# Kernel tuning notes

Measured on AMD Instinct MI355X. Metric: run time of the kernel, lower is better.

## Reference

```python
import jax, jax.numpy as jnp
import numpy as np

N = 100000   # nodes
E = 300000   # directed edges
NG = 4096    # graphs in batch
F_IN = 22
HID = 128


def setup_inputs() -> dict:
    key = jax.random.key(0)
    ks = jax.random.split(key, 32)
    s = 0.05
    inp = {
        "x": jax.random.normal(ks[0], (N, F_IN), jnp.float32),
        "edge_index": jax.random.randint(ks[1], (2, E), 0, N),
        "batch": jnp.sort(jax.random.randint(ks[2], (N,), 0, NG)),
        # GAT layer 1: 22 -> 4 heads x 32
        "W1": jax.random.normal(ks[3], (F_IN, HID), jnp.float32) * s,
        "as1": jax.random.normal(ks[4], (4, 32), jnp.float32) * s,
        "ad1": jax.random.normal(ks[5], (4, 32), jnp.float32) * s,
        "b1": jnp.zeros((HID,), jnp.float32),
        "g1": jnp.ones((HID,), jnp.float32),
        "be1": jnp.zeros((HID,), jnp.float32),
        # GAT layer 2: 128 -> 4 heads x 32
        "W2": jax.random.normal(ks[6], (HID, HID), jnp.float32) * s,
        "as2": jax.random.normal(ks[7], (4, 32), jnp.float32) * s,
        "ad2": jax.random.normal(ks[8], (4, 32), jnp.float32) * s,
        "b2": jnp.zeros((HID,), jnp.float32),
        "g2": jnp.ones((HID,), jnp.float32),
        "be2": jnp.zeros((HID,), jnp.float32),
        # GAT layer 3: 128 -> 1 head x 128
        "W3": jax.random.normal(ks[9], (HID, HID), jnp.float32) * s,
        "as3": jax.random.normal(ks[10], (1, HID), jnp.float32) * s,
        "ad3": jax.random.normal(ks[11], (1, HID), jnp.float32) * s,
        "b3": jnp.zeros((HID,), jnp.float32),
        "g3": jnp.ones((HID,), jnp.float32),
        "be3": jnp.zeros((HID,), jnp.float32),
        # MLP head
        "fw1": jax.random.normal(ks[12], (HID, 64), jnp.float32) * s,
        "fb1": jnp.zeros((64,), jnp.float32),
        "fw2": jax.random.normal(ks[13], (64, 1), jnp.float32) * s,
        "fb2": jnp.zeros((1,), jnp.float32),
    }
    return inp


def reference(x, edge_index, batch, W1, as1, ad1, b1, g1, be1,
              W2, as2, ad2, b2, g2, be2, W3, as3, ad3, b3, g3, be3,
              fw1, fb1, fw2, fb2):
    n = x.shape[0]
    sl = jnp.arange(n)
    src = jnp.concatenate([edge_index[0], sl])  # PyG GATConv adds self-loops
    dst = jnp.concatenate([edge_index[1], sl])

    def gat(h_in, W, a_s, a_d, b):
        H, C = a_s.shape
        h = (h_in @ W).reshape(n, H, C)                      # [N,H,C]
        al_s = jnp.einsum('nhc,hc->nh', h, a_s)              # per-node src score
        al_d = jnp.einsum('nhc,hc->nh', h, a_d)
        e = jax.nn.leaky_relu(al_s[src] + al_d[dst], 0.2)    # [Etot,H]
        emax = jax.ops.segment_max(e, dst, num_segments=n)
        ex = jnp.exp(e - emax[dst])
        den = jax.ops.segment_sum(ex, dst, num_segments=n)
        alpha = ex / (den[dst] + 1e-16)                       # segment softmax over in-edges
        msg = h[src] * alpha[:, :, None]                      # [Etot,H,C]
        out = jax.ops.segment_sum(msg, dst, num_segments=n)
        return out.reshape(n, H * C) + b

    def bn(h, g, be):
        m = h.mean(0)
        v = h.var(0)
        return (h - m) * jax.lax.rsqrt(v + 1e-5) * g + be

    h = jax.nn.relu(bn(gat(x, W1, as1, ad1, b1), g1, be1))
    h = jax.nn.relu(bn(gat(h, W2, as2, ad2, b2), g2, be2))
    h = jax.nn.relu(bn(gat(h, W3, as3, ad3, b3), g3, be3))

    # global mean pool over graphs
    s = jax.ops.segment_sum(h, batch, num_segments=NG)
    cnt = jax.ops.segment_sum(jnp.ones((n,), h.dtype), batch, num_segments=NG)
    pooled = s / jnp.maximum(cnt, 1.0)[:, None]

    z = jax.nn.relu(pooled @ fw1 + fb1)
    return z @ fw2 + fb2
```

## Files before the change

kernel.cpp:

```cpp
#include <hip/hip_runtime.h>

#define N_NODES 100000
#define N_EDGES 300000
#define N_ETOT  400000
#define NGRAPH  4096
#define HID     128
#define NBLK_SCAN 391
#define PNPB    32
#define STATS_BLOCKS 512
#define NSLICE  16

typedef __attribute__((ext_vector_type(8))) short short8;
typedef __attribute__((ext_vector_type(8))) ushort ushort8;
typedef __attribute__((ext_vector_type(4))) float f32x4;

__device__ __forceinline__ ushort f2bf(float f) {
    union { float f; unsigned u; } x; x.f = f;
    unsigned r = x.u + 0x7FFF + ((x.u >> 16) & 1);
    return (ushort)(r >> 16);
}

__device__ __forceinline__ float bf2f(ushort v) {
    union { unsigned u; float f; } t;
    t.u = ((unsigned)v) << 16;
    return t.f;
}

__device__ __forceinline__ float2 bf2f2(unsigned v) {
    union { unsigned u; float f; } lo, hi;
    lo.u = v << 16;
    hi.u = v & 0xFFFF0000u;
    return make_float2(lo.f, hi.f);
}

#define SETUP_W      36864
#define SETUP_SUMS   (SETUP_W + 3 * NSLICE * 256)
#define SETUP_CNTS   (SETUP_SUMS + N_NODES)
#define SETUP_TOT    (SETUP_CNTS + NGRAPH * HID + NGRAPH)
__global__ __launch_bounds__(256) void setup_kernel(
    const float* __restrict__ W1, const float* __restrict__ W2, const float* __restrict__ W3,
    ushort* __restrict__ Wt1, ushort* __restrict__ Wt2, ushort* __restrict__ Wt3,
    float* __restrict__ sums_base, int* __restrict__ counts,
    float* __restrict__ pooled)
{
    const int i = blockIdx.x * 256 + threadIdx.x;
    if (i < 16384) {
        int c = i >> 7, k = i & 127;
        Wt2[c * 128 + k] = f2bf(W2[k * 128 + c]);
    } else if (i < 32768) {
        int j = i - 16384; int c = j >> 7, k = j & 127;
        Wt3[c * 128 + k] = f2bf(W3[k * 128 + c]);
    } else if (i < SETUP_W) {
        int j = i - 32768; int c = j >> 5, k = j & 31;
        Wt1[c * 32 + k] = (k < 22) ? f2bf(W1[k * 128 + c]) : (ushort)0;
    } else if (i < SETUP_SUMS) {
        sums_base[i - SETUP_W] = 0.f;
    } else if (i < SETUP_CNTS) {
        counts[i - SETUP_SUMS] = 0;
    } else if (i < SETUP_TOT) {
        pooled[i - SETUP_CNTS] = 0.f;
    }
}

template<int K, bool PRE_BN, int HH, bool DX>
__global__ __launch_bounds__(256) void mfma_gemm_kernel(
    const ushort* __restrict__ Ab, const float* __restrict__ Af,
    const ushort* __restrict__ Wt,
    const float* __restrict__ sums, const float* __restrict__ g, const float* __restrict__ be,
    const float* __restrict__ avs, const float* __restrict__ avd,
    ushort* __restrict__ Cb, float* __restrict__ als, float* __restrict__ ald, int M)
{
    constexpr int SEGS = K / 8;
    constexpr int SSH  = (K == 128) ? 4 : 2;
    constexpr int SWM  = SEGS - 1;
    constexpr int NPB  = SEGS / 2;
    constexpr int KT   = K / 32;

    __shared__ ushort Bsm[128 * K];
    __shared__ float scsh[256];

    const int tid  = threadIdx.x;
    const int wave = tid >> 6;
    const int lane = tid & 63;
    const int ln   = lane & 15;
    const int quad = lane >> 4;
    const int r0   = blockIdx.x * 64 + wave * 16;
    const int ra   = r0 + ln;

    short8 wR[NPB];
    #pragma unroll
    for (int q = 0; q < NPB; ++q) {
        const int chunk = tid + q * 256;
        const int r   = chunk >> SSH;
        const int seg = chunk & SWM;
        wR[q] = *(const short8*)&Wt[(size_t)r * K + seg * 8];
    }
    short8 aF[KT];
    #pragma unroll
    for (int kt = 0; kt < KT; ++kt) {
        if constexpr (DX) {
            const int rr = min(ra, N_NODES - 1);
            #pragma unroll
            for (int i = 0; i < 8; ++i) {
                const int c = kt * 32 + quad * 8 + i;
                const float f = (c < 22) ? Af[(size_t)rr * 22 + c] : 0.f;
                aF[kt][i] = (short)f2bf(f);
            }
        } else {
            aF[kt] = *(const short8*)&Ab[(size_t)ra * K + kt * 32 + quad * 8];
        }
    }
    if constexpr (PRE_BN) {
        if (tid < 128) {
            float s = 0.f, q2 = 0.f;
            for (int b = 0; b < NSLICE; ++b) {
                s  += sums[b * 256 + tid];
                q2 += sums[b * 256 + 128 + tid];
            }
            const float m  = s * (1.f / N_NODES);
            const float v  = q2 * (1.f / N_NODES) - m * m;
            const float sc = g[tid] * rsqrtf(v + 1e-5f);
            scsh[tid]       = sc;
            scsh[tid + 128] = be[tid] - m * sc;
        }
    }
    #pragma unroll
    for (int q = 0; q < NPB; ++q) {
        const int chunk = tid + q * 256;
        const int r   = chunk >> SSH;
        const int seg = chunk & SWM;
        const int sp  = seg ^ (r & SWM);
        *(short8*)&Bsm[r * K + sp * 8] = wR[q];
    }
    __syncthreads();

    if constexpr (PRE_BN) {
        #pragma unroll
        for (int kt = 0; kt < KT; ++kt) {
            const int c0 = kt * 32 + quad * 8;
            #pragma unroll
            for (int i = 0; i < 8; ++i) {
                float f = bf2f((ushort)aF[kt][i]);
                f = fmaxf(f * scsh[c0 + i] + scsh[128 + c0 + i], 0.f);
                aF[kt][i] = (short)f2bf(f);
            }
        }
    }

    f32x4 acc[8] = {};
    #pragma unroll
    for (int kt = 0; kt < KT; ++kt) {
        #pragma unroll
        for (int tc = 0; tc < 8; ++tc) {
            const int ca = tc * 16 + ln;
            const short8 b = *(const short8*)&Bsm[ca * K + (((kt * 4 + quad) ^ (ca & SWM)) * 8)];
            acc[tc] = __builtin_amdgcn_mfma_f32_16x16x32_bf16(aF[kt], b, acc[tc], 0, 0, 0);
        }
    }

    #pragma unroll
    for (int rg = 0; rg < 4; ++rg) {
        const int gr = r0 + quad * 4 + rg;
        if (gr < M) {
            #pragma unroll
            for (int tc = 0; tc < 8; ++tc)
                Cb[(size_t)gr * HID + tc * 16 + ln] = f2bf(acc[tc][rg]);
        }
    }

    float avsr[8], avdr[8];
    #pragma unroll
    for (int tc = 0; tc < 8; ++tc) {
        avsr[tc] = avs[tc * 16 + ln];
        avdr[tc] = avd[tc * 16 + ln];
    }
    #pragma unroll
    for (int rg = 0; rg < 4; ++rg) {
        const int gr = r0 + quad * 4 + rg;
        float s[4], d[4];
        #pragma unroll
        for (int h = 0; h < 4; ++h) {
            float sv = 0.f, dv = 0.f;
            sv += acc[2 * h][rg] * avsr[2 * h];
            sv += acc[2 * h + 1][rg] * avsr[2 * h + 1];
            dv += acc[2 * h][rg] * avdr[2 * h];
            dv += acc[2 * h + 1][rg] * avdr[2 * h + 1];
            s[h] = sv; d[h] = dv;
        }
        #pragma unroll
        for (int m = 1; m < 16; m <<= 1) {
            #pragma unroll
            for (int h = 0; h < 4; ++h) {
                s[h] += __shfl_xor(s[h], m);
                d[h] += __shfl_xor(d[h], m);
            }
        }
        if (ln == 0 && gr < M) {
            if (HH == 4) {
                #pragma unroll
                for (int h = 0; h < 4; ++h) {
                    als[gr * 4 + h] = s[h];
                    ald[gr * 4 + h] = d[h];
                }
            } else {
                als[gr] = ((s[0] + s[1]) + s[2]) + s[3];
                ald[gr] = ((d[0] + d[1]) + d[2]) + d[3];
            }
        }
    }
}

__global__ void hist_kernel(const int* __restrict__ ei, int* __restrict__ counts) {
    int e = blockIdx.x * blockDim.x + threadIdx.x;
    if (e >= N_ETOT) return;
    int dst = (e < N_EDGES) ? ei[N_EDGES + e] : e - N_EDGES;
    atomicAdd(&counts[dst], 1);
}

__global__ __launch_bounds__(256) void scanA_kernel(
    const int* __restrict__ counts, int* __restrict__ rowptr, int* __restrict__ bsum)
{
    __shared__ int ls[256];
    const int t = threadIdx.x;
    const int i = blockIdx.x * 256 + t;
    const int v = (i < N_NODES) ? counts[i] : 0;
    ls[t] = v; __syncthreads();
    #pragma unroll
    for (int off = 1; off < 256; off <<= 1) {
        int add = (t >= off) ? ls[t - off] : 0;
        __syncthreads();
        ls[t] += add;
        __syncthreads();
    }
    if (i < N_NODES) rowptr[i] = ls[t] - v;
    if (t == 255) bsum[blockIdx.x] = ls[255];
}

__global__ __launch_bounds__(256) void scanC_kernel(
    int* __restrict__ rowptr, const int* __restrict__ bsum, int* __restrict__ cursor)
{
    __shared__ int red[256];
    const int t = threadIdx.x;
    int s = 0;
    for (int b = t; b < (int)blockIdx.x; b += 256) s += bsum[b];
    red[t] = s;
    __syncthreads();
    #pragma unroll
    for (int off = 128; off; off >>= 1) {
        if (t < off) red[t] += red[t + off];
        __syncthreads();
    }
    const int base = red[0];
    const int i = blockIdx.x * 256 + t;
    if (i < N_NODES) {
        const int v = rowptr[i] + base;
        rowptr[i] = v;
        cursor[i] = v;
    }
    if (i == 0) rowptr[N_NODES] = N_ETOT;
}

__global__ void scatter_kernel(const int* __restrict__ ei, int* __restrict__ cursor,
                               int* __restrict__ psrc)
{
    int e = blockIdx.x * blockDim.x + threadIdx.x;
    if (e >= N_ETOT) return;
    int src, dst;
    if (e < N_EDGES) { src = ei[e]; dst = ei[N_EDGES + e]; }
    else             { src = dst = e - N_EDGES; }
    int pos = atomicAdd(&cursor[dst], 1);
    psrc[pos] = src;
}

template<int HH>
__global__ __launch_bounds__(256) void agg_kernel(
    const ushort* __restrict__ H, const float* __restrict__ als,
    const float* __restrict__ ald, const int* __restrict__ rowptr,
    const int* __restrict__ psrc, ushort* __restrict__ Outb)
{
    const int tid   = threadIdx.x;
    const int w     = tid >> 6;
    const int lane  = tid & 63;
    const int grp   = lane >> 4;
    const int cl    = lane & 15;
    const int hd    = (HH == 4) ? (cl >> 2) : 0;
    const int nodeA = blockIdx.x * 8 + w * 2;
    const int nodeB = nodeA + 1;

    const int r0A = rowptr[nodeA];
    const int r1A = rowptr[nodeA + 1];
    const int r1B = rowptr[nodeB + 1];
    const float aldA = (HH == 4) ? ald[nodeA * 4 + hd] : ald[nodeA];
    const float aldB = (HH == 4) ? ald[nodeB * 4 + hd] : ald[nodeB];

    float denA = 0.f, denB = 0.f;
    float accA[8] = {}, accB[8] = {};
    int pA = r0A + grp;
    int pB = r1A + grp;
    bool aA = pA < r1A;
    bool aB = pB < r1B;
    int sA = psrc[aA ? pA : (r1A - 1)];
    int sB = psrc[aB ? pB : (r1B - 1)];
    while (pA < r1A || pB < r1B) {
        const float svA = (HH == 4) ? als[sA * 4 + hd] : als[sA];
        const float svB = (HH == 4) ? als[sB * 4 + hd] : als[sB];
        const uint4 hvA = *(const uint4*)&H[(size_t)sA * HID + cl * 8];
        const uint4 hvB = *(const uint4*)&H[(size_t)sB * HID + cl * 8];
        const int pA2 = pA + 4, pB2 = pB + 4;
        const bool aA2 = pA2 < r1A;
        const bool aB2 = pB2 < r1B;
        const int sA2 = psrc[aA2 ? pA2 : (r1A - 1)];
        const int sB2 = psrc[aB2 ? pB2 : (r1B - 1)];

        float vA = svA + aldA; vA = (vA > 0.f) ? vA : 0.2f * vA;
        float vB = svB + aldB; vB = (vB > 0.f) ? vB : 0.2f * vB;
        const float exA = aA ? __expf(vA) : 0.f;
        const float exB = aB ? __expf(vB) : 0.f;
        {
            const float2 h0 = bf2f2(hvA.x), h1 = bf2f2(hvA.y);
            const float2 h2 = bf2f2(hvA.z), h3 = bf2f2(hvA.w);
            accA[0] += exA * h0.x; accA[1] += exA * h0.y;
            accA[2] += exA * h1.x; accA[3] += exA * h1.y;
            accA[4] += exA * h2.x; accA[5] += exA * h2.y;
            accA[6] += exA * h3.x; accA[7] += exA * h3.y;
            denA += exA;
        }
        {
            const float2 h0 = bf2f2(hvB.x), h1 = bf2f2(hvB.y);
            const float2 h2 = bf2f2(hvB.z), h3 = bf2f2(hvB.w);
            accB[0] += exB * h0.x; accB[1] += exB * h0.y;
            accB[2] += exB * h1.x; accB[3] += exB * h1.y;
            accB[4] += exB * h2.x; accB[5] += exB * h2.y;
            accB[6] += exB * h3.x; accB[7] += exB * h3.y;
            denB += exB;
        }
        pA = pA2; pB = pB2;
        aA = aA2; aB = aB2;
        sA = sA2; sB = sB2;
    }
    #pragma unroll
    for (int m = 16; m < 64; m <<= 1) {
        denA += __shfl_xor(denA, m);
        denB += __shfl_xor(denB, m);
        #pragma unroll
        for (int i = 0; i < 8; ++i) {
            accA[i] += __shfl_xor(accA[i], m);
            accB[i] += __shfl_xor(accB[i], m);
        }
    }
    if (grp == 0) {
        const float inv = 1.f / (denA + 1e-16f);
        ushort8 o;
        #pragma unroll
        for (int i = 0; i < 8; ++i) o[i] = f2bf(accA[i] * inv);
        *(ushort8*)&Outb[(size_t)nodeA * HID + cl * 8] = o;
    } else if (grp == 1) {
        const float inv = 1.f / (denB + 1e-16f);
        ushort8 o;
        #pragma unroll
        for (int i = 0; i < 8; ++i) o[i] = f2bf(accB[i] * inv);
        *(ushort8*)&Outb[(size_t)nodeB * HID + cl * 8] = o;
    }
}

__global__ __launch_bounds__(256) void bn_stats_kernel(
    const ushort* __restrict__ X, float* __restrict__ sums_sl)
{
    __shared__ float ls[16][128], lq[16][128];
    const int tid = threadIdx.x;
    const int ro  = tid >> 4;
    const int ci  = tid & 15;
    const int c0  = ci * 8;
    const int rpb = (N_NODES + STATS_BLOCKS - 1) / STATS_BLOCKS;
    const int r0  = blockIdx.x * rpb;
    const int r1  = min(r0 + rpb, N_NODES);

    float s[8] = {}, q[8] = {};
    for (int r = r0 + ro; r < r1; r += 16) {
        const ushort8 v = *(const ushort8*)&X[(size_t)r * HID + c0];
        #pragma unroll
        for (int j = 0; j < 8; ++j) {
            const float f = bf2f(v[j]);
            s[j] += f; q[j] += f * f;
        }
    }
    #pragma unroll
    for (int j = 0; j < 8; ++j) { ls[ro][c0 + j] = s[j]; lq[ro][c0 + j] = q[j]; }
    __syncthreads();
    const int half = tid >> 7;
    const int c    = tid & 127;
    float acc = 0.f;
    if (half == 0) {
        #pragma unroll
        for (int k = 0; k < 16; ++k) acc += ls[k][c];
    } else {
        #pragma unroll
        for (int k = 0; k < 16; ++k) acc += lq[k][c];
    }
    atomicAdd(&sums_sl[(blockIdx.x & (NSLICE - 1)) * 256 + tid], acc);
}

__global__ __launch_bounds__(128) void bn_pool_kernel(
    const ushort* __restrict__ X,
    const float* __restrict__ sums, const float* __restrict__ g, const float* __restrict__ be,
    const int* __restrict__ batch, float* __restrict__ pooled, float* __restrict__ cnt)
{
    const int c = threadIdx.x;
    float s = 0.f, q2 = 0.f;
    for (int b = 0; b < NSLICE; ++b) {
        s  += sums[b * 256 + c];
        q2 += sums[b * 256 + 128 + c];
    }
    const float m  = s * (1.f / N_NODES);
    const float vv = q2 * (1.f / N_NODES) - m * m;
    const float sc = g[c] * rsqrtf(vv + 1e-5f);
    const float sh = be[c] - m * sc;

    const int n0 = blockIdx.x * PNPB;
    const int n1 = min(n0 + PNPB, N_NODES);
    int gcur = batch[n0];
    float acc = 0.f;
    int run = 0;
    for (int n = n0; n < n1; ++n) {
        const int gg = batch[n];
        if (gg != gcur) {
            atomicAdd(&pooled[(size_t)gcur * HID + c], acc);
            if (c == 0) atomicAdd(&cnt[gcur], (float)run);
            acc = 0.f; run = 0; gcur = gg;
        }
        const float v = bf2f(X[(size_t)n * HID + c]) * sc + sh;
        acc += fmaxf(v, 0.f);
        ++run;
    }
    atomicAdd(&pooled[(size_t)gcur * HID + c], acc);
    if (c == 0) atomicAdd(&cnt[gcur], (float)run);
}

__global__ __launch_bounds__(256) void mlp_kernel(
    const float* __restrict__ pooled, const float* __restrict__ cnt,
    const float* __restrict__ fw1, const float* __restrict__ fb1,
    const float* __restrict__ fw2, const float* __restrict__ fb2,
    float* __restrict__ out)
{
    __shared__ float w1[HID * 64];
    __shared__ float rows[4][HID];
    const int tid = threadIdx.x;
    for (int i = tid; i < HID * 64; i += 256) w1[i] = fw1[i];
    const int gl = tid >> 6;
    const int j  = tid & 63;
    const float b1 = fb1[j];
    const float w2 = fw2[j];
    __syncthreads();
    #pragma unroll
    for (int it = 0; it < 4; ++it) {
        const int g = blockIdx.x * 16 + it * 4 + gl;
        const float inv = 1.f / fmaxf(cnt[g], 1.f);
        rows[gl][j]      = pooled[(size_t)g * HID + j] * inv;
        rows[gl][j + 64] = pooled[(size_t)g * HID + 64 + j] * inv;
        __syncthreads();
        float z = b1;
        #pragma unroll 8
        for (int c2 = 0; c2 < HID; ++c2) z += rows[gl][c2] * w1[c2 * 64 + j];
        z = fmaxf(z, 0.f);
        float p = z * w2;
        #pragma unroll
        for (int off = 32; off; off >>= 1) p += __shfl_down(p, off);
        if (j == 0) out[g] = p + fb2[0];
        __syncthreads();
    }
}

extern "C" void kernel_launch(void* const* d_in, const int* in_sizes, int n_in,
                              void* d_out, int out_size, void* d_ws, size_t ws_size,
                              hipStream_t stream)
{
    const float* x     = (const float*)d_in[0];
    const int*   ei    = (const int*)d_in[1];
    const int*   batch = (const int*)d_in[2];
    const float* W1  = (const float*)d_in[3];
    const float* as1 = (const float*)d_in[4];
    const float* ad1 = (const float*)d_in[5];
    const float* g1  = (const float*)d_in[7];
    const float* be1 = (const float*)d_in[8];
    const float* W2  = (const float*)d_in[9];
    const float* as2 = (const float*)d_in[10];
    const float* ad2 = (const float*)d_in[11];
    const float* g2  = (const float*)d_in[13];
    const float* be2 = (const float*)d_in[14];
    const float* W3  = (const float*)d_in[15];
    const float* as3 = (const float*)d_in[16];
    const float* ad3 = (const float*)d_in[17];
    const float* g3  = (const float*)d_in[19];
    const float* be3 = (const float*)d_in[20];
    const float* fw1 = (const float*)d_in[21];
    const float* fb1 = (const float*)d_in[22];
    const float* fw2 = (const float*)d_in[23];
    const float* fb2 = (const float*)d_in[24];
    float* out = (float*)d_out;

    ushort* Hb  = (ushort*)d_ws;
    ushort* Bh  = Hb  + (size_t)N_NODES * HID;
    ushort* Wt1 = Bh  + (size_t)N_NODES * HID + 128 * 128;
    ushort* Wt2 = Wt1 + 128 * 32;
    ushort* Wt3 = Wt2 + 128 * 128;
    float* als    = (float*)(Wt3 + 128 * 128);
    float* ald    = als + (size_t)N_NODES * 4;
    float* sums1  = ald + (size_t)N_NODES * 4;
    float* sums2  = sums1 + NSLICE * 256;
    float* sums3  = sums2 + NSLICE * 256;
    float* pooled = sums3 + NSLICE * 256;
    float* cnt    = pooled + (size_t)NGRAPH * HID;
    int*   rowptr = (int*)(cnt + NGRAPH);
    int*   counts = rowptr + (N_NODES + 1);
    int*   cursor = counts + N_NODES;
    int*   bsum   = cursor + N_NODES;
    int*   psrc   = bsum + 512;

    auto cdiv = [](int a, int b) { return (a + b - 1) / b; };

    setup_kernel<<<cdiv(SETUP_TOT, 256), 256, 0, stream>>>(
        W1, W2, W3, Wt1, Wt2, Wt3, sums1, counts, pooled);

    hist_kernel<<<cdiv(N_ETOT, 256), 256, 0, stream>>>(ei, counts);
    scanA_kernel<<<NBLK_SCAN, 256, 0, stream>>>(counts, rowptr, bsum);
    scanC_kernel<<<NBLK_SCAN, 256, 0, stream>>>(rowptr, bsum, cursor);
    scatter_kernel<<<cdiv(N_ETOT, 256), 256, 0, stream>>>(ei, cursor, psrc);

    const int ggrid = cdiv(N_NODES, 64);
    const int agrid = N_NODES / 8;

    mfma_gemm_kernel<32, false, 4, true><<<ggrid, 256, 0, stream>>>(
        nullptr, x, Wt1, nullptr, nullptr, nullptr, as1, ad1, Hb, als, ald, N_NODES);
    agg_kernel<4><<<agrid, 256, 0, stream>>>(Hb, als, ald, rowptr, psrc, Bh);
    bn_stats_kernel<<<STATS_BLOCKS, 256, 0, stream>>>(Bh, sums1);

    mfma_gemm_kernel<128, true, 4, false><<<ggrid, 256, 0, stream>>>(
        Bh, nullptr, Wt2, sums1, g1, be1, as2, ad2, Hb, als, ald, N_NODES);
    agg_kernel<4><<<agrid, 256, 0, stream>>>(Hb, als, ald, rowptr, psrc, Bh);
    bn_stats_kernel<<<STATS_BLOCKS, 256, 0, stream>>>(Bh, sums2);

    mfma_gemm_kernel<128, true, 1, false><<<ggrid, 256, 0, stream>>>(
        Bh, nullptr, Wt3, sums2, g2, be2, as3, ad3, Hb, als, ald, N_NODES);
    agg_kernel<1><<<agrid, 256, 0, stream>>>(Hb, als, ald, rowptr, psrc, Bh);
    bn_stats_kernel<<<STATS_BLOCKS, 256, 0, stream>>>(Bh, sums3);

    bn_pool_kernel<<<cdiv(N_NODES, PNPB), 128, 0, stream>>>(
        Bh, sums3, g3, be3, batch, pooled, cnt);
    mlp_kernel<<<NGRAPH / 16, 256, 0, stream>>>(pooled, cnt, fw1, fb1, fw2, fb2, out);
}
```

Before: 319.9 us.

## Fuse BN statistics into following GEMM and pool kernels via grid barriers

Removes the three standalone bn_stats kernels. The BN statistics are now computed inside the next GEMM and inside the pooling kernel, each of which runs as a persistent grid and uses a software grid barrier before applying the normalization. This saves three launches and lets the persistent blocks keep the reduced stats, at the cost of a spin-wait barrier. That barrier relies on every block being co-resident (768 GEMM blocks with launch bounds of 3 per SM, 1024 pool blocks), so it risks deadlock or stalls if occupancy is lower than assumed.

```diff
diff --git a/kernel.cpp b/kernel.cpp
--- a/kernel.cpp
+++ b/kernel.cpp
@@ -7,8 +7,10 @@
 #define HID     128
 #define NBLK_SCAN 391
 #define PNPB    32
-#define STATS_BLOCKS 512
+#define NCHUNK  3125
 #define NSLICE  16
+#define GEMM_BN_GRID 768
+#define POOL_GRID   1024
 
 typedef __attribute__((ext_vector_type(8))) short short8;
 typedef __attribute__((ext_vector_type(8))) ushort ushort8;
@@ -33,14 +35,28 @@
     return make_float2(lo.f, hi.f);
 }
 
+__device__ __forceinline__ float aload(float* p) {
+    return __hip_atomic_load(p, __ATOMIC_RELAXED, __HIP_MEMORY_SCOPE_AGENT);
+}
+
+__device__ __forceinline__ void grid_barrier(int* bar, int nblk) {
+    __syncthreads();
+    if (threadIdx.x == 0) {
+        __hip_atomic_fetch_add(bar, 1, __ATOMIC_RELAXED, __HIP_MEMORY_SCOPE_AGENT);
+        while (__hip_atomic_load(bar, __ATOMIC_RELAXED, __HIP_MEMORY_SCOPE_AGENT) < nblk) {}
+    }
+    __syncthreads();
+}
+
 #define SETUP_W      36864
 #define SETUP_SUMS   (SETUP_W + 3 * NSLICE * 256)
-#define SETUP_CNTS   (SETUP_SUMS + N_NODES)
+#define SETUP_BARS   (SETUP_SUMS + 4)
+#define SETUP_CNTS   (SETUP_BARS + N_NODES)
 #define SETUP_TOT    (SETUP_CNTS + NGRAPH * HID + NGRAPH)
 __global__ __launch_bounds__(256) void setup_kernel(
     const float* __restrict__ W1, const float* __restrict__ W2, const float* __restrict__ W3,
     ushort* __restrict__ Wt1, ushort* __restrict__ Wt2, ushort* __restrict__ Wt3,
-    float* __restrict__ sums_base, int* __restrict__ counts,
+    float* __restrict__ sums_base, int* __restrict__ bars, int* __restrict__ counts,
     float* __restrict__ pooled)
 {
     const int i = blockIdx.x * 256 + threadIdx.x;
@@ -55,20 +71,23 @@
         Wt1[c * 32 + k] = (k < 22) ? f2bf(W1[k * 128 + c]) : (ushort)0;
     } else if (i < SETUP_SUMS) {
         sums_base[i - SETUP_W] = 0.f;
+    } else if (i < SETUP_BARS) {
+        bars[i - SETUP_SUMS] = 0;
     } else if (i < SETUP_CNTS) {
-        counts[i - SETUP_SUMS] = 0;
+        counts[i - SETUP_BARS] = 0;
     } else if (i < SETUP_TOT) {
         pooled[i - SETUP_CNTS] = 0.f;
     }
 }
 
 template<int K, bool PRE_BN, int HH, bool DX>
-__global__ __launch_bounds__(256) void mfma_gemm_kernel(
+__global__ __launch_bounds__(256, 3) void mfma_gemm_kernel(
     const ushort* __restrict__ Ab, const float* __restrict__ Af,
     const ushort* __restrict__ Wt,
-    const float* __restrict__ sums, const float* __restrict__ g, const float* __restrict__ be,
+    float* __restrict__ sums, const float* __restrict__ g, const float* __restrict__ be,
     const float* __restrict__ avs, const float* __restrict__ avd,
-    ushort* __restrict__ Cb, float* __restrict__ als, float* __restrict__ ald, int M)
+    ushort* __restrict__ Cb, float* __restrict__ als, float* __restrict__ ald, int M,
+    int* __restrict__ bar, int nblk)
 {
     constexpr int SEGS = K / 8;
     constexpr int SSH  = (K == 128) ? 4 : 2;
@@ -84,89 +103,82 @@
     const int lane = tid & 63;
     const int ln   = lane & 15;
     const int quad = lane >> 4;
-    const int r0   = blockIdx.x * 64 + wave * 16;
-    const int ra   = r0 + ln;
+    const int NT   = (M + 63) >> 6;
+
+    if constexpr (PRE_BN) {
+        const int ro = tid >> 4;
+        const int c0 = (tid & 15) * 8;
+        float s[8] = {}, q[8] = {};
+        for (int t = blockIdx.x; t < NT; t += gridDim.x) {
+            #pragma unroll
+            for (int rr = 0; rr < 4; ++rr) {
+                const int row = t * 64 + ro + rr * 16;
+                if (row < M) {
+                    const ushort8 v = *(const ushort8*)&Ab[(size_t)row * K + c0];
+                    #pragma unroll
+                    for (int j = 0; j < 8; ++j) {
+                        const float f = bf2f(v[j]);
+                        s[j] += f; q[j] += f * f;
+                    }
+                }
+            }
+        }
+        float* ls = (float*)Bsm;
+        float* lq = ls + 16 * 128;
+        #pragma unroll
+        for (int j = 0; j < 8; ++j) { ls[ro * 128 + c0 + j] = s[j]; lq[ro * 128 + c0 + j] = q[j]; }
+        __syncthreads();
+        {
+            const int half = tid >> 7;
+            const int c    = tid & 127;
+            float acc = 0.f;
+            if (half == 0) {
+                #pragma unroll
+                for (int k = 0; k < 16; ++k) acc += ls[k * 128 + c];
+            } else {
+                #pragma unroll
+                for (int k = 0; k < 16; ++k) acc += lq[k * 128 + c];
+            }
+            atomicAdd(&sums[(blockIdx.x & (NSLICE - 1)) * 256 + tid], acc);
+        }
+    }
 
     short8 wR[NPB];
     #pragma unroll
-    for (int q = 0; q < NPB; ++q) {
-        const int chunk = tid + q * 256;
+    for (int p = 0; p < NPB; ++p) {
+        const int chunk = tid + p * 256;
         const int r   = chunk >> SSH;
         const int seg = chunk & SWM;
-        wR[q] = *(const short8*)&Wt[(size_t)r * K + seg * 8];
-    }
-    short8 aF[KT];
-    #pragma unroll
-    for (int kt = 0; kt < KT; ++kt) {
-        if constexpr (DX) {
-            const int rr = min(ra, N_NODES - 1);
-            #pragma unroll
-            for (int i = 0; i < 8; ++i) {
-                const int c = kt * 32 + quad * 8 + i;
-                const float f = (c < 22) ? Af[(size_t)rr * 22 + c] : 0.f;
-                aF[kt][i] = (short)f2bf(f);
-            }
-        } else {
-            aF[kt] = *(const short8*)&Ab[(size_t)ra * K + kt * 32 + quad * 8];
-        }
+        wR[p] = *(const short8*)&Wt[(size_t)r * K + seg * 8];
+    }
+
+    if constexpr (PRE_BN) {
+        grid_barrier(bar, nblk);
+    }
+
+    #pragma unroll
+    for (int p = 0; p < NPB; ++p) {
+        const int chunk = tid + p * 256;
+        const int r   = chunk >> SSH;
+        const int seg = chunk & SWM;
+        const int sp  = seg ^ (r & SWM);
+        *(short8*)&Bsm[r * K + sp * 8] = wR[p];
     }
     if constexpr (PRE_BN) {
         if (tid < 128) {
-            float s = 0.f, q2 = 0.f;
+            float ss = 0.f, qq = 0.f;
             for (int b = 0; b < NSLICE; ++b) {
-                s  += sums[b * 256 + tid];
-                q2 += sums[b * 256 + 128 + tid];
-            }
-            const float m  = s * (1.f / N_NODES);
-            const float v  = q2 * (1.f / N_NODES) - m * m;
+                ss += aload(&sums[b * 256 + tid]);
+                qq += aload(&sums[b * 256 + 128 + tid]);
+            }
+            const float m  = ss * (1.f / N_NODES);
+            const float v  = qq * (1.f / N_NODES) - m * m;
             const float sc = g[tid] * rsqrtf(v + 1e-5f);
             scsh[tid]       = sc;
             scsh[tid + 128] = be[tid] - m * sc;
         }
     }
-    #pragma unroll
-    for (int q = 0; q < NPB; ++q) {
-        const int chunk = tid + q * 256;
-        const int r   = chunk >> SSH;
-        const int seg = chunk & SWM;
-        const int sp  = seg ^ (r & SWM);
-        *(short8*)&Bsm[r * K + sp * 8] = wR[q];
-    }
     __syncthreads();
-
-    if constexpr (PRE_BN) {
-        #pragma unroll
-        for (int kt = 0; kt < KT; ++kt) {
-            const int c0 = kt * 32 + quad * 8;
-            #pragma unroll
-            for (int i = 0; i < 8; ++i) {
-                float f = bf2f((ushort)aF[kt][i]);
-                f = fmaxf(f * scsh[c0 + i] + scsh[128 + c0 + i], 0.f);
-                aF[kt][i] = (short)f2bf(f);
-            }
-        }
-    }
-
-    f32x4 acc[8] = {};
-    #pragma unroll
-    for (int kt = 0; kt < KT; ++kt) {
-        #pragma unroll
-        for (int tc = 0; tc < 8; ++tc) {
-            const int ca = tc * 16 + ln;
-            const short8 b = *(const short8*)&Bsm[ca * K + (((kt * 4 + quad) ^ (ca & SWM)) * 8)];
-            acc[tc] = __builtin_amdgcn_mfma_f32_16x16x32_bf16(aF[kt], b, acc[tc], 0, 0, 0);
-        }
-    }
-
-    #pragma unroll
-    for (int rg = 0; rg < 4; ++rg) {
-        const int gr = r0 + quad * 4 + rg;
-        if (gr < M) {
-            #pragma unroll
-            for (int tc = 0; tc < 8; ++tc)
-                Cb[(size_t)gr * HID + tc * 16 + ln] = f2bf(acc[tc][rg]);
-        }
-    }
 
     float avsr[8], avdr[8];
     #pragma unroll
@@ -174,37 +186,92 @@
         avsr[tc] = avs[tc * 16 + ln];
         avdr[tc] = avd[tc * 16 + ln];
     }
-    #pragma unroll
-    for (int rg = 0; rg < 4; ++rg) {
-        const int gr = r0 + quad * 4 + rg;
-        float s[4], d[4];
-        #pragma unroll
-        for (int h = 0; h < 4; ++h) {
-            float sv = 0.f, dv = 0.f;
-            sv += acc[2 * h][rg] * avsr[2 * h];
-            sv += acc[2 * h + 1][rg] * avsr[2 * h + 1];
-            dv += acc[2 * h][rg] * avdr[2 * h];
-            dv += acc[2 * h + 1][rg] * avdr[2 * h + 1];
-            s[h] = sv; d[h] = dv;
-        }
-        #pragma unroll
-        for (int m = 1; m < 16; m <<= 1) {
+
+    for (int t = blockIdx.x; t < NT; t += gridDim.x) {
+        const int r0 = t * 64 + wave * 16;
+        const int ra = r0 + ln;
+
+        short8 aF[KT];
+        #pragma unroll
+        for (int kt = 0; kt < KT; ++kt) {
+            if constexpr (DX) {
+                const int rr = min(ra, N_NODES - 1);
+                #pragma unroll
+                for (int i = 0; i < 8; ++i) {
+                    const int c = kt * 32 + quad * 8 + i;
+                    const float f = (c < 22) ? Af[(size_t)rr * 22 + c] : 0.f;
+                    aF[kt][i] = (short)f2bf(f);
+                }
+            } else {
+                aF[kt] = *(const short8*)&Ab[(size_t)ra * K + kt * 32 + quad * 8];
+            }
+        }
+        if constexpr (PRE_BN) {
+            #pragma unroll
+            for (int kt = 0; kt < KT; ++kt) {
+                const int c0 = kt * 32 + quad * 8;
+                #pragma unroll
+                for (int i = 0; i < 8; ++i) {
+                    float f = bf2f((ushort)aF[kt][i]);
+                    f = fmaxf(f * scsh[c0 + i] + scsh[128 + c0 + i], 0.f);
+                    aF[kt][i] = (short)f2bf(f);
+                }
+            }
+        }
+
+        f32x4 acc[8] = {};
+        #pragma unroll
+        for (int kt = 0; kt < KT; ++kt) {
+            #pragma unroll
+            for (int tc = 0; tc < 8; ++tc) {
+                const int ca = tc * 16 + ln;
+                const short8 b = *(const short8*)&Bsm[ca * K + (((kt * 4 + quad) ^ (ca & SWM)) * 8)];
+                acc[tc] = __builtin_amdgcn_mfma_f32_16x16x32_bf16(aF[kt], b, acc[tc], 0, 0, 0);
+            }
+        }
+
+        #pragma unroll
+        for (int rg = 0; rg < 4; ++rg) {
+            const int gr = r0 + quad * 4 + rg;
+            if (gr < M) {
+                #pragma unroll
+                for (int tc = 0; tc < 8; ++tc)
+                    Cb[(size_t)gr * HID + tc * 16 + ln] = f2bf(acc[tc][rg]);
+            }
+        }
+
+        #pragma unroll
+        for (int rg = 0; rg < 4; ++rg) {
+            const int gr = r0 + quad * 4 + rg;
+            float s[4], d[4];
             #pragma unroll
             for (int h = 0; h < 4; ++h) {
-                s[h] += __shfl_xor(s[h], m);
-                d[h] += __shfl_xor(d[h], m);
-            }
-        }
-        if (ln == 0 && gr < M) {
-            if (HH == 4) {
+                float sv = 0.f, dv = 0.f;
+                sv += acc[2 * h][rg] * avsr[2 * h];
+                sv += acc[2 * h + 1][rg] * avsr[2 * h + 1];
+                dv += acc[2 * h][rg] * avdr[2 * h];
+                dv += acc[2 * h + 1][rg] * avdr[2 * h + 1];
+                s[h] = sv; d[h] = dv;
+            }
+            #pragma unroll
+            for (int m = 1; m < 16; m <<= 1) {
                 #pragma unroll
                 for (int h = 0; h < 4; ++h) {
-                    als[gr * 4 + h] = s[h];
-                    ald[gr * 4 + h] = d[h];
+                    s[h] += __shfl_xor(s[h], m);
+                    d[h] += __shfl_xor(d[h], m);
                 }
-            } else {
-                als[gr] = ((s[0] + s[1]) + s[2]) + s[3];
-                ald[gr] = ((d[0] + d[1]) + d[2]) + d[3];
+            }
+            if (ln == 0 && gr < M) {
+                if (HH == 4) {
+                    #pragma unroll
+                    for (int h = 0; h < 4; ++h) {
+                        als[gr * 4 + h] = s[h];
+                        ald[gr * 4 + h] = d[h];
+                    }
+                } else {
+                    als[gr] = ((s[0] + s[1]) + s[2]) + s[3];
+                    ald[gr] = ((d[0] + d[1]) + d[2]) + d[3];
+                }
             }
         }
     }
@@ -363,77 +430,56 @@
     }
 }
 
-__global__ __launch_bounds__(256) void bn_stats_kernel(
-    const ushort* __restrict__ X, float* __restrict__ sums_sl)
-{
-    __shared__ float ls[16][128], lq[16][128];
-    const int tid = threadIdx.x;
-    const int ro  = tid >> 4;
-    const int ci  = tid & 15;
-    const int c0  = ci * 8;
-    const int rpb = (N_NODES + STATS_BLOCKS - 1) / STATS_BLOCKS;
-    const int r0  = blockIdx.x * rpb;
-    const int r1  = min(r0 + rpb, N_NODES);
-
-    float s[8] = {}, q[8] = {};
-    for (int r = r0 + ro; r < r1; r += 16) {
-        const ushort8 v = *(const ushort8*)&X[(size_t)r * HID + c0];
-        #pragma unroll
-        for (int j = 0; j < 8; ++j) {
-            const float f = bf2f(v[j]);
-            s[j] += f; q[j] += f * f;
-        }
-    }
-    #pragma unroll
-    for (int j = 0; j < 8; ++j) { ls[ro][c0 + j] = s[j]; lq[ro][c0 + j] = q[j]; }
-    __syncthreads();
-    const int half = tid >> 7;
-    const int c    = tid & 127;
-    float acc = 0.f;
-    if (half == 0) {
-        #pragma unroll
-        for (int k = 0; k < 16; ++k) acc += ls[k][c];
-    } else {
-        #pragma unroll
-        for (int k = 0; k < 16; ++k) acc += lq[k][c];
-    }
-    atomicAdd(&sums_sl[(blockIdx.x & (NSLICE - 1)) * 256 + tid], acc);
-}
-
-__global__ __launch_bounds__(128) void bn_pool_kernel(
+__global__ __launch_bounds__(128, 2) void bn_pool_kernel(
     const ushort* __restrict__ X,
-    const float* __restrict__ sums, const float* __restrict__ g, const float* __restrict__ be,
-    const int* __restrict__ batch, float* __restrict__ pooled, float* __restrict__ cnt)
+    float* __restrict__ sums, const float* __restrict__ g, const float* __restrict__ be,
+    const int* __restrict__ batch, float* __restrict__ pooled, float* __restrict__ cnt,
+    int* __restrict__ bar)
 {
     const int c = threadIdx.x;
-    float s = 0.f, q2 = 0.f;
+    float s = 0.f, q = 0.f;
+    for (int ch = blockIdx.x; ch < NCHUNK; ch += gridDim.x) {
+        const int n0 = ch * PNPB;
+        const int n1 = min(n0 + PNPB, N_NODES);
+        for (int n = n0; n < n1; ++n) {
+            const float f = bf2f(X[(size_t)n * HID + c]);
+            s += f; q += f * f;
+        }
+    }
+    atomicAdd(&sums[(blockIdx.x & (NSLICE - 1)) * 256 + c], s);
+    atomicAdd(&sums[(blockIdx.x & (NSLICE - 1)) * 256 + 128 + c], q);
+    grid_barrier(bar, gridDim.x);
+
+    float ss = 0.f, qq = 0.f;
     for (int b = 0; b < NSLICE; ++b) {
-        s  += sums[b * 256 + c];
-        q2 += sums[b * 256 + 128 + c];
-    }
-    const float m  = s * (1.f / N_NODES);
-    const float vv = q2 * (1.f / N_NODES) - m * m;
+        ss += aload(&sums[b * 256 + c]);
+        qq += aload(&sums[b * 256 + 128 + c]);
+    }
+    const float m  = ss * (1.f / N_NODES);
+    const float vv = qq * (1.f / N_NODES) - m * m;
     const float sc = g[c] * rsqrtf(vv + 1e-5f);
     const float sh = be[c] - m * sc;
 
-    const int n0 = blockIdx.x * PNPB;
-    const int n1 = min(n0 + PNPB, N_NODES);
-    int gcur = batch[n0];
-    float acc = 0.f;
-    int run = 0;
-    for (int n = n0; n < n1; ++n) {
-        const int gg = batch[n];
-        if (gg != gcur) {
-            atomicAdd(&pooled[(size_t)gcur * HID + c], acc);
-            if (c == 0) atomicAdd(&cnt[gcur], (float)run);
-            acc = 0.f; run = 0; gcur = gg;
-        }
-        const float v = bf2f(X[(size_t)n * HID + c]) * sc + sh;
-        acc += fmaxf(v, 0.f);
-        ++run;
-    }
-    atomicAdd(&pooled[(size_t)gcur * HID + c], acc);
-    if (c == 0) atomicAdd(&cnt[gcur], (float)run);
+    for (int ch = blockIdx.x; ch < NCHUNK; ch += gridDim.x) {
+        const int n0 = ch * PNPB;
+        const int n1 = min(n0 + PNPB, N_NODES);
+        int gcur = batch[n0];
+        float acc = 0.f;
+        int run = 0;
+        for (int n = n0; n < n1; ++n) {
+            const int gg = batch[n];
+            if (gg != gcur) {
+                atomicAdd(&pooled[(size_t)gcur * HID + c], acc);
+                if (c == 0) atomicAdd(&cnt[gcur], (float)run);
+                acc = 0.f; run = 0; gcur = gg;
+            }
+            const float v = bf2f(X[(size_t)n * HID + c]) * sc + sh;
+            acc += fmaxf(v, 0.f);
+            ++run;
+        }
+        atomicAdd(&pooled[(size_t)gcur * HID + c], acc);
+        if (c == 0) atomicAdd(&cnt[gcur], (float)run);
+    }
 }
 
 __global__ __launch_bounds__(256) void mlp_kernel(
@@ -508,7 +554,8 @@
     float* sums1  = ald + (size_t)N_NODES * 4;
     float* sums2  = sums1 + NSLICE * 256;
     float* sums3  = sums2 + NSLICE * 256;
-    float* pooled = sums3 + NSLICE * 256;
+    int*   bars   = (int*)(sums3 + NSLICE * 256);
+    float* pooled = (float*)(bars + 4);
     float* cnt    = pooled + (size_t)NGRAPH * HID;
     int*   rowptr = (int*)(cnt + NGRAPH);
     int*   counts = rowptr + (N_NODES + 1);
@@ -519,7 +566,7 @@
     auto cdiv = [](int a, int b) { return (a + b - 1) / b; };
 
     setup_kernel<<<cdiv(SETUP_TOT, 256), 256, 0, stream>>>(
-        W1, W2, W3, Wt1, Wt2, Wt3, sums1, counts, pooled);
+        W1, W2, W3, Wt1, Wt2, Wt3, sums1, bars, counts, pooled);
 
     hist_kernel<<<cdiv(N_ETOT, 256), 256, 0, stream>>>(ei, counts);
     scanA_kernel<<<NBLK_SCAN, 256, 0, stream>>>(counts, rowptr, bsum);
@@ -530,21 +577,21 @@
     const int agrid = N_NODES / 8;
 
     mfma_gemm_kernel<32, false, 4, true><<<ggrid, 256, 0, stream>>>(
-        nullptr, x, Wt1, nullptr, nullptr, nullptr, as1, ad1, Hb, als, ald, N_NODES);
+        nullptr, x, Wt1, nullptr, nullptr, nullptr, as1, ad1, Hb, als, ald, N_NODES,
+        nullptr, 0);
     agg_kernel<4><<<agrid, 256, 0, stream>>>(Hb, als, ald, rowptr, psrc, Bh);
-    bn_stats_kernel<<<STATS_BLOCKS, 256, 0, stream>>>(Bh, sums1);
-
-    mfma_gemm_kernel<128, true, 4, false><<<ggrid, 256, 0, stream>>>(
-        Bh, nullptr, Wt2, sums1, g1, be1, as2, ad2, Hb, als, ald, N_NODES);
+
+    mfma_gemm_kernel<128, true, 4, false><<<GEMM_BN_GRID, 256, 0, stream>>>(
+        Bh, nullptr, Wt2, sums1, g1, be1, as2, ad2, Hb, als, ald, N_NODES,
+        bars + 0, GEMM_BN_GRID);
     agg_kernel<4><<<agrid, 256, 0, stream>>>(Hb, als, ald, rowptr, psrc, Bh);
-    bn_stats_kernel<<<STATS_BLOCKS, 256, 0, stream>>>(Bh, sums2);
-
-    mfma_gemm_kernel<128, true, 1, false><<<ggrid, 256, 0, stream>>>(
-        Bh, nullptr, Wt3, sums2, g2, be2, as3, ad3, Hb, als, ald, N_NODES);
+
+    mfma_gemm_kernel<128, true, 1, false><<<GEMM_BN_GRID, 256, 0, stream>>>(
+        Bh, nullptr, Wt3, sums2, g2, be2, as3, ad3, Hb, als, ald, N_NODES,
+        bars + 1, GEMM_BN_GRID);
     agg_kernel<1><<<agrid, 256, 0, stream>>>(Hb, als, ald, rowptr, psrc, Bh);
-    bn_stats_kernel<<<STATS_BLOCKS, 256, 0, stream>>>(Bh, sums3);
-
-    bn_pool_kernel<<<cdiv(N_NODES, PNPB), 128, 0, stream>>>(
-        Bh, sums3, g3, be3, batch, pooled, cnt);
+
+    bn_pool_kernel<<<POOL_GRID, 128, 0, stream>>>(
+        Bh, sums3, g3, be3, batch, pooled, cnt, bars + 2);
     mlp_kernel<<<NGRAPH / 16, 256, 0, stream>>>(pooled, cnt, fw1, fb1, fw2, fb2, out);
 }
```

After: 558.5 us. 74.6% more time.
